# Kernel tuning notes

Hardware: AMD Instinct MI355X
Metric: run time of the kernel (lower is better)

## Reference

```python
import jax, jax.numpy as jnp
import numpy as np

B, T, D, H = 32, 8192, 128, 128

def setup_inputs() -> dict:
    key = jax.random.key(0)
    k1, k2, k3, k4, k5 = jax.random.split(key, 5)
    return {
        "encoder_outputs": jax.random.normal(k1, (B, T, D), dtype=jnp.float32),
        "decoder_hidden": jax.random.normal(k2, (B, H), dtype=jnp.float32),
        "W1": jax.random.normal(k3, (D, D), dtype=jnp.float32) * 0.08,
        "W2": jax.random.normal(k4, (H, D), dtype=jnp.float32) * 0.08,
        "V": jax.random.normal(k5, (D, 1), dtype=jnp.float32) * 0.08,
    }

def reference(encoder_outputs, decoder_hidden, W1, W2, V):
    # score: [B, T, D] = tanh(enc @ W1 + (dec @ W2)[:, None, :])
    score = jnp.tanh(jnp.einsum('btd,de->bte', encoder_outputs, W1)
                     + jnp.einsum('bh,hd->bd', decoder_hidden, W2)[:, None, :])
    # logits: [B, T, 1]; softmax over time axis (axis=1)
    logits = jnp.einsum('btd,do->bto', score, V)
    attention_weights = jax.nn.softmax(logits, axis=1)
    # context: [B, D] weighted sum over T
    context_vector = jnp.sum(attention_weights * encoder_outputs, axis=1)
    return context_vector, attention_weights
```

## Files before the change

### kernel.cpp

```cpp
#include <hip/hip_runtime.h>

#define B_ 32
#define T_ 8192
#define D_ 128
#define MBLK 128
#define NCHUNK 64

typedef __attribute__((ext_vector_type(8))) _Float16 half8;
typedef __attribute__((ext_vector_type(4))) _Float16 half4;
typedef __attribute__((ext_vector_type(4))) float floatx4;

__device__ __forceinline__ float tanh_fast(float x) {
    float e = __expf(2.0f * x);
    return 1.0f - __fdividef(2.0f, e + 1.0f);
}

__global__ void prep_kernel(const float* __restrict__ W1, half8* __restrict__ W1frag,
                            const float* __restrict__ dec, const float* __restrict__ W2,
                            float* __restrict__ bias) {
    int bid = blockIdx.x, tid = threadIdx.x;
    if (bid < 8) {
        int tg = bid * 256 + tid;
        int kk = tg >> 9, ni = (tg >> 6) & 7, lane = tg & 63;
        half8 h;
        #pragma unroll
        for (int j = 0; j < 8; ++j) {
            int k = kk * 32 + ((lane >> 4) * 8) + j;
            int n = ni * 16 + (lane & 15);
            h[j] = (_Float16)W1[k * 128 + n];
        }
        W1frag[tg] = h;
    } else {
        int b = (bid - 8) * 2 + (tid >> 7);
        int d = tid & 127;
        float acc = 0.f;
        for (int h = 0; h < 128; ++h)
            acc += dec[b * 128 + h] * W2[h * 128 + d];
        bias[b * 128 + d] = acc;
    }
}

__global__ __launch_bounds__(256)
void main_kernel(const float* __restrict__ enc, const half8* __restrict__ W1frag,
                 const float* __restrict__ bias, const float* __restrict__ V,
                 float* __restrict__ out_w, float* __restrict__ m_part,
                 float* __restrict__ s_part, float* __restrict__ c_part)
{
    __shared__ __align__(16) _Float16 encl[MBLK * 128];
    __shared__ __align__(16) half8 bfr[2048];
    __shared__ float red[MBLK];
    __shared__ float c_red[8 * 128];

    const int tid = threadIdx.x;
    const int l = tid & 63;
    const int w = tid >> 6;
    const int bid = blockIdx.x;
    const int b = bid >> 6;
    const int chunk = bid & 63;
    const float* encp = enc + ((long)(b * T_) + chunk * MBLK) * D_;

    #pragma unroll
    for (int q = 0; q < 8; ++q)
        bfr[q * 256 + tid] = W1frag[q * 256 + tid];

    #pragma unroll
    for (int q = 0; q < 16; ++q) {
        int flat = (q * 256 + tid) * 4;
        int r = flat >> 7, c = flat & 127;
        float4 f = *(const float4*)(encp + flat);
        half4 h;
        h[0] = (_Float16)f.x; h[1] = (_Float16)f.y;
        h[2] = (_Float16)f.z; h[3] = (_Float16)f.w;
        int byte = r * 256 + ((c * 2) ^ ((r & 7) << 4));
        *(half4*)((char*)encl + byte) = h;
    }
    __syncthreads();

    floatx4 acc[2][8];
    #pragma unroll
    for (int si = 0; si < 2; ++si)
        #pragma unroll
        for (int ni = 0; ni < 8; ++ni) acc[si][ni] = (floatx4)0.0f;

    const int arow = w * 32 + (l & 15);
    const int asw = (arow & 7) << 4;
    #pragma unroll
    for (int kk = 0; kk < 4; ++kk) {
        int koff = (kk * 64 + ((l >> 4) * 16)) ^ asw;
        half8 a0 = *(const half8*)((char*)encl + (arow * 256 + koff));
        half8 a1 = *(const half8*)((char*)encl + ((arow + 16) * 256 + koff));
        #pragma unroll
        for (int ni = 0; ni < 8; ++ni) {
            half8 bf = bfr[(kk * 8 + ni) * 64 + l];
            acc[0][ni] = __builtin_amdgcn_mfma_f32_16x16x32_f16(a0, bf, acc[0][ni], 0, 0, 0);
            acc[1][ni] = __builtin_amdgcn_mfma_f32_16x16x32_f16(a1, bf, acc[1][ni], 0, 0, 0);
        }
    }

    float bs[8], vv[8];
    #pragma unroll
    for (int ni = 0; ni < 8; ++ni) {
        int n = ni * 16 + (l & 15);
        bs[ni] = bias[b * 128 + n];
        vv[ni] = V[n];
    }
    #pragma unroll
    for (int si = 0; si < 2; ++si) {
        #pragma unroll
        for (int j2 = 0; j2 < 4; ++j2) {
            float p = 0.f;
            #pragma unroll
            for (int ni = 0; ni < 8; ++ni)
                p += tanh_fast(acc[si][ni][j2] + bs[ni]) * vv[ni];
            #pragma unroll
            for (int mk = 1; mk < 16; mk <<= 1)
                p += __shfl_xor(p, mk);
            if ((l & 15) == 0) {
                int r = w * 32 + si * 16 + (l >> 4) * 4 + j2;
                red[r] = p;
                out_w[(long)b * T_ + chunk * MBLK + r] = p;
            }
        }
    }
    __syncthreads();

    if (tid < 64) {
        float l0 = red[tid], l1 = red[tid + 64];
        float m = fmaxf(l0, l1);
        #pragma unroll
        for (int mk = 1; mk < 64; mk <<= 1) m = fmaxf(m, __shfl_xor(m, mk));
        float e0 = __expf(l0 - m), e1 = __expf(l1 - m);
        float s = e0 + e1;
        #pragma unroll
        for (int mk = 1; mk < 64; mk <<= 1) s += __shfl_xor(s, mk);
        red[tid] = e0; red[tid + 64] = e1;
        if (tid == 0) { m_part[bid] = m; s_part[bid] = s; }
    }
    __syncthreads();

    {
        int c0 = (tid & 31) * 4, rg = tid >> 5;
        floatx4 cc = (floatx4)0.0f;
        #pragma unroll
        for (int rr = 0; rr < 16; ++rr) {
            int r = rg * 16 + rr;
            float wgt = red[r];
            half4 h = *(const half4*)((char*)encl +
                       (r * 256 + (((tid & 31) * 8) ^ ((r & 7) << 4))));
            #pragma unroll
            for (int i = 0; i < 4; ++i) cc[i] += wgt * (float)h[i];
        }
        *(floatx4*)(&c_red[rg * 128 + c0]) = cc;
    }
    __syncthreads();
    if (tid < 128) {
        float s = 0.f;
        #pragma unroll
        for (int g = 0; g < 8; ++g) s += c_red[g * 128 + tid];
        c_part[(long)bid * 128 + tid] = s;
    }
}

__global__ void reduce_kernel(const float* __restrict__ m_part, const float* __restrict__ s_part,
                              const float* __restrict__ c_part, float* __restrict__ ctx,
                              float* __restrict__ mg, float* __restrict__ sg)
{
    __shared__ float sm[64];
    __shared__ float sc[64];
    int b = blockIdx.x, i = threadIdx.x;
    float m = m_part[b * 64 + i];
    sm[i] = m;
    __syncthreads();
    for (int s = 32; s > 0; s >>= 1) {
        if (i < s) sm[i] = fmaxf(sm[i], sm[i + s]);
        __syncthreads();
    }
    float m_g = sm[0];
    __syncthreads();
    float e = __expf(m - m_g);
    sm[i] = s_part[b * 64 + i] * e;
    __syncthreads();
    for (int s = 32; s > 0; s >>= 1) {
        if (i < s) sm[i] += sm[i + s];
        __syncthreads();
    }
    float s_g = sm[0];
    __syncthreads();
    sc[i] = e / s_g;
    if (i == 0) { mg[b] = m_g; sg[b] = s_g; }
    __syncthreads();
    float acc0 = 0.f, acc1 = 0.f;
    for (int ch = 0; ch < 64; ++ch) {
        float w = sc[ch];
        acc0 += c_part[((long)b * 64 + ch) * 128 + i] * w;
        acc1 += c_part[((long)b * 64 + ch) * 128 + 64 + i] * w;
    }
    ctx[b * 128 + i] = acc0;
    ctx[b * 128 + 64 + i] = acc1;
}

__global__ void finalize_kernel(float* __restrict__ out_w, const float* __restrict__ mg,
                                const float* __restrict__ sg)
{
    int idx = blockIdx.x * 256 + threadIdx.x;
    int b = idx >> 13;
    float lg = out_w[idx];
    out_w[idx] = __expf(lg - mg[b]) / sg[b];
}

extern "C" void kernel_launch(void* const* d_in, const int* in_sizes, int n_in,
                              void* d_out, int out_size, void* d_ws, size_t ws_size,
                              hipStream_t stream)
{
    const float* enc = (const float*)d_in[0];
    const float* dec = (const float*)d_in[1];
    const float* W1  = (const float*)d_in[2];
    const float* W2  = (const float*)d_in[3];
    const float* V   = (const float*)d_in[4];

    float* ctx  = (float*)d_out;
    float* outw = ctx + B_ * D_;

    float* ws     = (float*)d_ws;
    float* bias   = ws;
    float* m_part = bias + 4096;
    float* s_part = m_part + 2048;
    float* mg     = s_part + 2048;
    float* sg     = mg + 32;
    float* c_part = sg + 32;
    half8* W1frag = (half8*)(c_part + (long)B_ * NCHUNK * 128);

    prep_kernel<<<24, 256, 0, stream>>>(W1, W1frag, dec, W2, bias);
    main_kernel<<<B_ * NCHUNK, 256, 0, stream>>>(enc, W1frag, bias, V, outw, m_part, s_part, c_part);
    reduce_kernel<<<B_, 64, 0, stream>>>(m_part, s_part, c_part, ctx, mg, sg);
    finalize_kernel<<<(B_ * T_) / 256, 256, 0, stream>>>(outw, mg, sg);
}
```

Measured before the change: 58.45 us.

## Use 512-thread blocks with register-resident A fragments and fewer barriers

Doubles main_kernel's block size to 512 threads (8 waves), so each wave handles 16 rows instead of 32. Each lane loads its A fragment straight from global memory into registers, runs the MFMAs without first staging through LDS, and only afterwards writes the fp16 rows to LDS for the context pass. Every wave now computes the block max itself, and the context pass recomputes the exponential weights inline, which removes one barrier and the single-wave softmax step. The cost is more exp calls per block, and the 512-thread, 4-block launch bound may constrain register allocation.

New measurement: 54.62 us. 6.5% less time.

```diff
diff --git a/kernel.cpp b/kernel.cpp
--- a/kernel.cpp
+++ b/kernel.cpp
@@ -40,7 +40,7 @@
     }
 }
 
-__global__ __launch_bounds__(256)
+__global__ __launch_bounds__(512, 4)
 void main_kernel(const float* __restrict__ enc, const half8* __restrict__ W1frag,
                  const float* __restrict__ bias, const float* __restrict__ V,
                  float* __restrict__ out_w, float* __restrict__ m_part,
@@ -49,7 +49,7 @@
     __shared__ __align__(16) _Float16 encl[MBLK * 128];
     __shared__ __align__(16) half8 bfr[2048];
     __shared__ float red[MBLK];
-    __shared__ float c_red[8 * 128];
+    __shared__ float c_red[16][128];
 
     const int tid = threadIdx.x;
     const int l = tid & 63;
@@ -60,40 +60,42 @@
     const float* encp = enc + ((long)(b * T_) + chunk * MBLK) * D_;
 
     #pragma unroll
-    for (int q = 0; q < 8; ++q)
-        bfr[q * 256 + tid] = W1frag[q * 256 + tid];
-
-    #pragma unroll
-    for (int q = 0; q < 16; ++q) {
-        int flat = (q * 256 + tid) * 4;
-        int r = flat >> 7, c = flat & 127;
-        float4 f = *(const float4*)(encp + flat);
-        half4 h;
-        h[0] = (_Float16)f.x; h[1] = (_Float16)f.y;
-        h[2] = (_Float16)f.z; h[3] = (_Float16)f.w;
-        int byte = r * 256 + ((c * 2) ^ ((r & 7) << 4));
-        *(half4*)((char*)encl + byte) = h;
-    }
-    __syncthreads();
-
-    floatx4 acc[2][8];
-    #pragma unroll
-    for (int si = 0; si < 2; ++si)
-        #pragma unroll
-        for (int ni = 0; ni < 8; ++ni) acc[si][ni] = (floatx4)0.0f;
-
-    const int arow = w * 32 + (l & 15);
-    const int asw = (arow & 7) << 4;
+    for (int q = 0; q < 4; ++q)
+        bfr[q * 512 + tid] = W1frag[q * 512 + tid];
+
+    const int arow = w * 16 + (l & 15);
+    const float* rowp = encp + arow * 128 + ((l >> 4) * 8);
+    half8 afr[4];
     #pragma unroll
     for (int kk = 0; kk < 4; ++kk) {
-        int koff = (kk * 64 + ((l >> 4) * 16)) ^ asw;
-        half8 a0 = *(const half8*)((char*)encl + (arow * 256 + koff));
-        half8 a1 = *(const half8*)((char*)encl + ((arow + 16) * 256 + koff));
-        #pragma unroll
-        for (int ni = 0; ni < 8; ++ni) {
-            half8 bf = bfr[(kk * 8 + ni) * 64 + l];
-            acc[0][ni] = __builtin_amdgcn_mfma_f32_16x16x32_f16(a0, bf, acc[0][ni], 0, 0, 0);
-            acc[1][ni] = __builtin_amdgcn_mfma_f32_16x16x32_f16(a1, bf, acc[1][ni], 0, 0, 0);
+        float4 f0 = *(const float4*)(rowp + kk * 32);
+        float4 f1 = *(const float4*)(rowp + kk * 32 + 4);
+        half8 a;
+        a[0] = (_Float16)f0.x; a[1] = (_Float16)f0.y;
+        a[2] = (_Float16)f0.z; a[3] = (_Float16)f0.w;
+        a[4] = (_Float16)f1.x; a[5] = (_Float16)f1.y;
+        a[6] = (_Float16)f1.z; a[7] = (_Float16)f1.w;
+        afr[kk] = a;
+    }
+    __syncthreads();
+
+    floatx4 acc[8];
+    #pragma unroll
+    for (int ni = 0; ni < 8; ++ni) acc[ni] = (floatx4)0.0f;
+
+    #pragma unroll
+    for (int kk = 0; kk < 4; ++kk)
+        #pragma unroll
+        for (int ni = 0; ni < 8; ++ni)
+            acc[ni] = __builtin_amdgcn_mfma_f32_16x16x32_f16(
+                          afr[kk], bfr[(kk * 8 + ni) * 64 + l], acc[ni], 0, 0, 0);
+
+    {
+        const int asw = (arow & 7) << 4;
+        #pragma unroll
+        for (int kk = 0; kk < 4; ++kk) {
+            int byte = arow * 256 + (((kk * 64) + ((l >> 4) * 16)) ^ asw);
+            *(half8*)((char*)encl + byte) = afr[kk];
         }
     }
 
@@ -105,58 +107,53 @@
         vv[ni] = V[n];
     }
     #pragma unroll
-    for (int si = 0; si < 2; ++si) {
-        #pragma unroll
-        for (int j2 = 0; j2 < 4; ++j2) {
-            float p = 0.f;
-            #pragma unroll
-            for (int ni = 0; ni < 8; ++ni)
-                p += tanh_fast(acc[si][ni][j2] + bs[ni]) * vv[ni];
-            #pragma unroll
-            for (int mk = 1; mk < 16; mk <<= 1)
-                p += __shfl_xor(p, mk);
-            if ((l & 15) == 0) {
-                int r = w * 32 + si * 16 + (l >> 4) * 4 + j2;
-                red[r] = p;
-                out_w[(long)b * T_ + chunk * MBLK + r] = p;
-            }
-        }
-    }
-    __syncthreads();
-
-    if (tid < 64) {
-        float l0 = red[tid], l1 = red[tid + 64];
-        float m = fmaxf(l0, l1);
-        #pragma unroll
-        for (int mk = 1; mk < 64; mk <<= 1) m = fmaxf(m, __shfl_xor(m, mk));
+    for (int j2 = 0; j2 < 4; ++j2) {
+        float p = 0.f;
+        #pragma unroll
+        for (int ni = 0; ni < 8; ++ni)
+            p += tanh_fast(acc[ni][j2] + bs[ni]) * vv[ni];
+        #pragma unroll
+        for (int mk = 1; mk < 16; mk <<= 1)
+            p += __shfl_xor(p, mk);
+        if ((l & 15) == 0) {
+            int r = w * 16 + (l >> 4) * 4 + j2;
+            red[r] = p;
+            out_w[(long)b * T_ + chunk * MBLK + r] = p;
+        }
+    }
+    __syncthreads();
+
+    float l0 = red[l], l1 = red[l + 64];
+    float m = fmaxf(l0, l1);
+    #pragma unroll
+    for (int mk = 1; mk < 64; mk <<= 1) m = fmaxf(m, __shfl_xor(m, mk));
+    {
         float e0 = __expf(l0 - m), e1 = __expf(l1 - m);
         float s = e0 + e1;
         #pragma unroll
         for (int mk = 1; mk < 64; mk <<= 1) s += __shfl_xor(s, mk);
-        red[tid] = e0; red[tid + 64] = e1;
         if (tid == 0) { m_part[bid] = m; s_part[bid] = s; }
     }
-    __syncthreads();
 
     {
-        int c0 = (tid & 31) * 4, rg = tid >> 5;
+        int dg = tid & 31, rg = tid >> 5;
         floatx4 cc = (floatx4)0.0f;
         #pragma unroll
-        for (int rr = 0; rr < 16; ++rr) {
-            int r = rg * 16 + rr;
-            float wgt = red[r];
+        for (int rr = 0; rr < 8; ++rr) {
+            int r = rg * 8 + rr;
+            float wgt = __expf(red[r] - m);
             half4 h = *(const half4*)((char*)encl +
-                       (r * 256 + (((tid & 31) * 8) ^ ((r & 7) << 4))));
+                       (r * 256 + ((dg * 8) ^ ((r & 7) << 4))));
             #pragma unroll
             for (int i = 0; i < 4; ++i) cc[i] += wgt * (float)h[i];
         }
-        *(floatx4*)(&c_red[rg * 128 + c0]) = cc;
+        *(floatx4*)(&c_red[rg][dg * 4]) = cc;
     }
     __syncthreads();
     if (tid < 128) {
         float s = 0.f;
         #pragma unroll
-        for (int g = 0; g < 8; ++g) s += c_red[g * 128 + tid];
+        for (int g = 0; g < 16; ++g) s += c_red[g][tid];
         c_part[(long)bid * 128 + tid] = s;
     }
 }
@@ -231,7 +228,7 @@
     half8* W1frag = (half8*)(c_part + (long)B_ * NCHUNK * 128);
 
     prep_kernel<<<24, 256, 0, stream>>>(W1, W1frag, dec, W2, bias);
-    main_kernel<<<B_ * NCHUNK, 256, 0, stream>>>(enc, W1frag, bias, V, outw, m_part, s_part, c_part);
+    main_kernel<<<B_ * NCHUNK, 512, 0, stream>>>(enc, W1frag, bias, V, outw, m_part, s_part, c_part);
     reduce_kernel<<<B_, 64, 0, stream>>>(m_part, s_part, c_part, ctx, mg, sg);
     finalize_kernel<<<(B_ * T_) / 256, 256, 0, stream>>>(outw, mg, sg);
 }
```
